# Kernel optimization log

Hardware: AMD Instinct MI355X
Metric: run time of the kernel (lower is better)

## Reference

```python
import jax, jax.numpy as jnp
import numpy as np

N_EMBED = 768
N_HEAD = 12
HEAD_DIM = N_EMBED // N_HEAD


def setup_inputs() -> dict:
    key = jax.random.key(0)
    k1, k2, k3, k4, k5 = jax.random.split(key, 5)
    B, T = 8, 1024
    x = jax.random.normal(k1, (B, T, N_EMBED), dtype=jnp.float32)
    s = 0.02
    W_attn = jax.random.normal(k2, (N_EMBED, 3 * N_EMBED), dtype=jnp.float32) * s
    b_attn = jnp.zeros((3 * N_EMBED,), dtype=jnp.float32)
    W_proj = jax.random.normal(k3, (N_EMBED, N_EMBED), dtype=jnp.float32) * s
    b_proj = jnp.zeros((N_EMBED,), dtype=jnp.float32)
    return {"x": x, "W_attn": W_attn, "b_attn": b_attn, "W_proj": W_proj, "b_proj": b_proj}


def reference(x, W_attn, b_attn, W_proj, b_proj):
    B, T, C = x.shape
    qkv = x @ W_attn + b_attn  # [B, T, 3C]
    q, k, v = jnp.split(qkv, 3, axis=-1)
    # [B, H, T, D]
    q = q.reshape(B, T, N_HEAD, HEAD_DIM).transpose(0, 2, 1, 3)
    k = k.reshape(B, T, N_HEAD, HEAD_DIM).transpose(0, 2, 1, 3)
    v = v.reshape(B, T, N_HEAD, HEAD_DIM).transpose(0, 2, 1, 3)
    scale = 1.0 / jnp.sqrt(jnp.asarray(HEAD_DIM, dtype=x.dtype))
    att = jnp.einsum('bhqd,bhkd->bhqk', q, k) * scale  # [B, H, T, T]
    causal = jnp.tril(jnp.ones((T, T), dtype=bool))
    att = jnp.where(causal[None, None], att, -jnp.inf)
    att = jax.nn.softmax(att, axis=-1)
    y = jnp.einsum('bhqk,bhkd->bhqd', att, v)  # [B, H, T, D]
    y = y.transpose(0, 2, 1, 3).reshape(B, T, C)
    return y @ W_proj + b_proj
```

## Files before the change

kernel.cpp:

```cpp
#include <hip/hip_runtime.h>

#define B_ 8
#define T_ 1024
#define C_ 768
#define H_ 12
#define D_ 64
#define M_ (B_*T_)
#define N3_ (3*C_)
#define NQK_ 1536

#define QSCALE 0.18033688011112042f
#define SXQ (127.0f/6.0f)
#define SWQ (127.0f/0.12f)
#define DEQ ((6.0f/127.0f)*(0.12f/127.0f))

typedef __bf16 bf16x8 __attribute__((ext_vector_type(8)));
typedef float f32x4 __attribute__((ext_vector_type(4)));
typedef int i32x4 __attribute__((ext_vector_type(4)));

__device__ __forceinline__ ushort f2bf(float f){
  __bf16 h = (__bf16)f;
  return __builtin_bit_cast(ushort, h);
}
__device__ __forceinline__ signed char q8(float f, float s){
  float v = rintf(f * s);
  v = fminf(fmaxf(v, -127.f), 127.f);
  return (signed char)(int)v;
}

__device__ __forceinline__ void gload_lds16(const void* g, void* l){
  __builtin_amdgcn_global_load_lds(
      (const __attribute__((address_space(1))) void*)g,
      (__attribute__((address_space(3))) void*)l, 16, 0, 0);
}

__global__ __launch_bounds__(256) void prep(const float* __restrict__ x, signed char* __restrict__ xq,
                     const float* __restrict__ Wa, signed char* __restrict__ Waq,
                     const float* __restrict__ Wp, ushort* __restrict__ WpT){
  const int bid = blockIdx.x, tid = threadIdx.x;
  if (bid < 1536){
    int i = (bid * 256 + tid) * 16;
    union { signed char c[16]; int4 v; } u;
    #pragma unroll
    for (int j = 0; j < 4; ++j){
      float4 f = *(const float4*)(x + i + j*4);
      u.c[j*4+0] = q8(f.x, SXQ); u.c[j*4+1] = q8(f.y, SXQ);
      u.c[j*4+2] = q8(f.z, SXQ); u.c[j*4+3] = q8(f.w, SXQ);
    }
    *(int4*)(xq + i) = u.v;
  } else if (bid < 3264){
    __shared__ float tile[32][33];
    int b2 = bid - 1536;
    int c0 = (b2 % 72) * 32, r0 = (b2 / 72) * 32;
    const int tx = tid & 31, ty = tid >> 5;
    for (int i = ty; i < 32; i += 8)
      tile[i][tx] = Wa[(size_t)(r0 + i) * N3_ + c0 + tx];
    __syncthreads();
    for (int i = ty; i < 32; i += 8)
      Waq[(size_t)(c0 + i) * C_ + r0 + tx] = q8(tile[tx][i], SWQ);
  } else {
    __shared__ float tile[32][33];
    int b2 = bid - 3264;
    int c0 = (b2 % 24) * 32, r0 = (b2 / 24) * 32;
    const int tx = tid & 31, ty = tid >> 5;
    for (int i = ty; i < 32; i += 8)
      tile[i][tx] = Wp[(size_t)(r0 + i) * C_ + c0 + tx];
    __syncthreads();
    for (int i = ty; i < 32; i += 8)
      WpT[(size_t)(c0 + i) * C_ + r0 + tx] = f2bf(tile[tx][i]);
  }
}

__global__ __launch_bounds__(256) void gemm_qkv_i8(const signed char* __restrict__ A,
                        const signed char* __restrict__ BT, const float* __restrict__ bias,
                        ushort* __restrict__ qk, ushort* __restrict__ Vt){
  __shared__ __align__(16) char smem8[34816];
  const int K = C_;
  const int tid = threadIdx.x;
  const int lane = tid & 63, w = tid >> 6;
  const int wr = w >> 1, wc = w & 1;
  const int lr = lane & 15, lg = lane >> 4;
  const int gdx = gridDim.x;
  const int total = gdx * gridDim.y;
  int id = blockIdx.y * gdx + blockIdx.x;
  int nid = (id & 7) * (total >> 3) + (id >> 3);
  const int m0 = (nid / gdx) * 128, n0 = (nid % gdx) * 128;
  i32x4 acc[4][4] = {};
  #define STAGE8(bf, k0s)                                                      \
    _Pragma("unroll")                                                          \
    for (int j = 0; j < 2; ++j){                                               \
      int idj = tid + j * 256;                                                 \
      int row = idj >> 2, sl = idj & 3;                                        \
      gload_lds16(&A [(size_t)(m0 + row) * K + (k0s) + sl * 16],               \
                  &smem8[(bf)*16384 + idj * 16]);                              \
      gload_lds16(&BT[(size_t)(n0 + row) * K + (k0s) + sl * 16],               \
                  &smem8[(bf)*16384 + 8192 + idj * 16]);                       \
    }
  STAGE8(0, 0)
  int cur = 0;
  for (int k0 = 0; k0 < K; k0 += 64){
    const bool more = (k0 + 64 < K);
    if (more) { STAGE8(cur ^ 1, k0 + 64) }
    __builtin_amdgcn_sched_barrier(0);
    if (more) asm volatile("s_waitcnt vmcnt(4)" ::: "memory");
    else      asm volatile("s_waitcnt vmcnt(0)" ::: "memory");
    __builtin_amdgcn_sched_barrier(0);
    __builtin_amdgcn_s_barrier();
    __builtin_amdgcn_sched_barrier(0);
    const char* Asb = &smem8[cur * 16384];
    const char* Bsb = &smem8[cur * 16384 + 8192];
    i32x4 af[4], bfr[4];
    #pragma unroll
    for (int m = 0; m < 4; ++m)
      af[m]  = *(const i32x4*)&Asb[(wr*64 + m*16 + lr) * 64 + lg * 16];
    #pragma unroll
    for (int n = 0; n < 4; ++n)
      bfr[n] = *(const i32x4*)&Bsb[(wc*64 + n*16 + lr) * 64 + lg * 16];
    __builtin_amdgcn_s_setprio(1);
    #pragma unroll
    for (int m = 0; m < 4; ++m)
      #pragma unroll
      for (int n = 0; n < 4; ++n)
        acc[m][n] = __builtin_amdgcn_mfma_i32_16x16x64_i8(af[m], bfr[n], acc[m][n], 0, 0, 0);
    __builtin_amdgcn_s_setprio(0);
    __builtin_amdgcn_sched_barrier(0);
    __builtin_amdgcn_s_barrier();
    __builtin_amdgcn_sched_barrier(0);
    cur ^= 1;
  }
  #undef STAGE8
  constexpr int LDC = 136;
  ushort* Ts = (ushort*)smem8;
  const bool isV = (n0 >= 2*C_);
  #pragma unroll
  for (int n = 0; n < 4; ++n){
    int cl = wc*64 + n*16 + lr;
    int col = n0 + cl;
    float bv = bias[col];
    float sc = (col < C_) ? QSCALE : 1.0f;
    if (isV){
      int rl = wr*64;
      #pragma unroll
      for (int m = 0; m < 4; ++m){
        ushort4 o;
        #pragma unroll
        for (int i = 0; i < 4; ++i)
          ((ushort*)&o)[i] = f2bf((float)acc[m][n][i] * DEQ + bv);
        *(ushort4*)&Ts[cl * LDC + rl + m*16 + lg*4] = o;
      }
    } else {
      #pragma unroll
      for (int m = 0; m < 4; ++m){
        int rl = wr*64 + m*16 + lg*4;
        #pragma unroll
        for (int i = 0; i < 4; ++i)
          Ts[(rl + i) * LDC + cl] = f2bf(((float)acc[m][n][i] * DEQ + bv) * sc);
      }
    }
  }
  __syncthreads();
  const int bb = m0 >> 10, tt = m0 & 1023;
  #pragma unroll
  for (int it = 0; it < 8; ++it){
    int idx = tid + it * 256;
    int rc = idx >> 4, sg = idx & 15;
    int4 v = *(const int4*)&Ts[rc * LDC + sg * 8];
    if (isV){
      int ch = n0 - 2*C_ + rc;
      int hh = ch >> 6, dd = ch & 63;
      *(int4*)&Vt[((size_t)(bb * H_ + hh) * 64 + dd) * 1024 + tt + sg * 8] = v;
    } else {
      *(int4*)&qk[(size_t)(m0 + rc) * NQK_ + n0 + sg * 8] = v;
    }
  }
}

__global__ __launch_bounds__(256) void gemm_proj(const ushort* __restrict__ A, const ushort* __restrict__ BT,
                        const float* __restrict__ bias, float* __restrict__ Cf32,
                        int M, int N, int K){
  __shared__ __align__(16) ushort smem[32768];
  const int tid = threadIdx.x;
  const int lane = tid & 63, w = tid >> 6;
  const int wr = w >> 1, wc = w & 1;
  const int lr = lane & 15, lg = lane >> 4;
  const int gdx = gridDim.x;
  const int total = gdx * gridDim.y;
  int id = blockIdx.y * gdx + blockIdx.x;
  int nid = (id & 7) * (total >> 3) + (id >> 3);
  const int m0 = (nid / gdx) * 128, n0 = (nid % gdx) * 128;
  f32x4 acc[4][4] = {};
  const int srow = lane >> 3;
  const int sseg = (lane & 7) ^ srow;
  #define STAGE(bf, k0s)                                                       \
    _Pragma("unroll")                                                          \
    for (int c = 0; c < 4; ++c){                                               \
      int row = w*32 + c*8 + srow;                                             \
      gload_lds16(&A [(size_t)(m0 + row) * K + (k0s) + sseg * 8],              \
                  &smem[(bf)*16384 + (w*32 + c*8) * 64]);                      \
      gload_lds16(&BT[(size_t)(n0 + row) * K + (k0s) + sseg * 8],              \
                  &smem[(bf)*16384 + 8192 + (w*32 + c*8) * 64]);               \
    }
  STAGE(0, 0)
  int cur = 0;
  for (int k0 = 0; k0 < K; k0 += 64){
    const bool more = (k0 + 64 < K);
    if (more) { STAGE(cur ^ 1, k0 + 64) }
    __builtin_amdgcn_sched_barrier(0);
    if (more) asm volatile("s_waitcnt vmcnt(8)" ::: "memory");
    else      asm volatile("s_waitcnt vmcnt(0)" ::: "memory");
    __builtin_amdgcn_sched_barrier(0);
    __builtin_amdgcn_s_barrier();
    __builtin_amdgcn_sched_barrier(0);
    const ushort* Asb = &smem[cur * 16384];
    const ushort* Bsb = &smem[cur * 16384 + 8192];
    #pragma unroll
    for (int kk = 0; kk < 64; kk += 32){
      bf16x8 af[4], bfr[4];
      #pragma unroll
      for (int m = 0; m < 4; ++m)
        af[m]  = *(const bf16x8*)&Asb[(wr*64 + m*16 + lr) * 64 + ((kk + lg*8) ^ ((lr & 7) << 3))];
      #pragma unroll
      for (int n = 0; n < 4; ++n)
        bfr[n] = *(const bf16x8*)&Bsb[(wc*64 + n*16 + lr) * 64 + ((kk + lg*8) ^ ((lr & 7) << 3))];
      #pragma unroll
      for (int m = 0; m < 4; ++m)
        #pragma unroll
        for (int n = 0; n < 4; ++n)
          acc[m][n] = __builtin_amdgcn_mfma_f32_16x16x32_bf16(af[m], bfr[n], acc[m][n], 0, 0, 0);
    }
    __builtin_amdgcn_sched_barrier(0);
    __builtin_amdgcn_s_barrier();
    __builtin_amdgcn_sched_barrier(0);
    cur ^= 1;
  }
  #undef STAGE
  #pragma unroll
  for (int n = 0; n < 4; ++n){
    int col = n0 + wc*64 + n*16 + lr;
    float bv = bias[col];
    #pragma unroll
    for (int m = 0; m < 4; ++m){
      int rowb = m0 + wr*64 + m*16 + lg*4;
      #pragma unroll
      for (int i = 0; i < 4; ++i)
        Cf32[(size_t)(rowb + i) * N + col] = acc[m][n][i] + bv;
    }
  }
}

__global__ __launch_bounds__(64, 4) void attn_fused(const ushort* __restrict__ qk,
                        const ushort* __restrict__ Vt, ushort* __restrict__ ya){
  __shared__ __align__(16) ushort Ks[2][4096];
  __shared__ __align__(16) ushort Vs[4096];
  __shared__ __align__(16) ushort Ps[32 * 36];
  const int lane = threadIdx.x & 63;
  const int lr = lane & 15, lg = lane >> 4;
  const int srow = lane >> 3;
  const int sseg = (lane & 7) ^ srow;
  const int bx = blockIdx.x;
  const int xcd = bx & 7, ii = bx >> 3;
  const int hi = ii % 12, s = ii / 12;
  const int bh = xcd * 12 + hi;
  const int b = bh / H_, h = bh % H_;
  const ushort* Kb = qk + (size_t)b * T_ * NQK_ + C_ + h * D_;
  const ushort* Vb = Vt + (size_t)bh * D_ * T_;

  int par = 0;
  for (int hf = 0; hf < 2; ++hf){
    const int qw = hf ? (31 - s) : s;
    bf16x8 qf[2][2];
    #pragma unroll
    for (int n = 0; n < 2; ++n){
      int qr = qw*32 + n*16 + lr;
      const ushort* qp = qk + ((size_t)(b * T_ + qr)) * NQK_ + h * D_;
      #pragma unroll
      for (int kk = 0; kk < 2; ++kk)
        qf[n][kk] = __builtin_bit_cast(bf16x8, *(const int4*)(qp + kk*32 + lg*8));
    }

    f32x4 yacc[4][2] = {};
    float lsum[2] = {0.f, 0.f};
    const int qwmin = qw*32;
    const int nktw = ((qwmin + 31) >> 6) + 1;
    #pragma unroll
    for (int c = 0; c < 8; ++c)
      gload_lds16(&Kb[(size_t)(c*8 + srow) * NQK_ + sseg * 8], &Ks[par][c * 512]);
    for (int kt = 0; kt < nktw; ++kt){
      const bool more = (kt + 1 < nktw);
      #pragma unroll
      for (int c = 0; c < 8; ++c)
        gload_lds16(&Vb[(size_t)(c*8 + srow) * T_ + kt*64 + sseg * 8], &Vs[c * 512]);
      if (more){
        #pragma unroll
        for (int c = 0; c < 8; ++c)
          gload_lds16(&Kb[(size_t)((kt+1)*64 + c*8 + srow) * NQK_ + sseg * 8], &Ks[par ^ 1][c * 512]);
        asm volatile("s_waitcnt vmcnt(16)" ::: "memory");
      } else {
        asm volatile("s_waitcnt vmcnt(8)" ::: "memory");
      }
      __builtin_amdgcn_sched_barrier(0);

      f32x4 st[4][2] = {};
      const ushort* Kc = Ks[par];
      #pragma unroll
      for (int kk = 0; kk < 2; ++kk){
        bf16x8 kf[4];
        #pragma unroll
        for (int m = 0; m < 4; ++m)
          kf[m] = *(const bf16x8*)&Kc[(m*16 + lr) * 64 + ((kk*32 + lg*8) ^ ((lr & 7) << 3))];
        __builtin_amdgcn_s_setprio(1);
        #pragma unroll
        for (int m = 0; m < 4; ++m)
          #pragma unroll
          for (int n = 0; n < 2; ++n)
            st[m][n] = __builtin_amdgcn_mfma_f32_16x16x32_bf16(kf[m], qf[n][kk], st[m][n], 0, 0, 0);
        __builtin_amdgcn_s_setprio(0);
      }

      const bool needmask = (kt*64 + 63 > qwmin);
      #pragma unroll
      for (int kkh = 0; kkh < 2; ++kkh){
        #pragma unroll
        for (int n = 0; n < 2; ++n){
          int q = qwmin + n*16 + lr;
          float ps = 0.f;
          #pragma unroll
          for (int mh = 0; mh < 2; ++mh){
            int m = kkh*2 + mh;
            ushort4 pk;
            #pragma unroll
            for (int i = 0; i < 4; ++i){
              float sv = st[m][n][i];
              if (needmask){
                int key = kt*64 + m*16 + lg*4 + i;
                sv = (key <= q) ? sv : -1e30f;
              }
              float p = __builtin_amdgcn_exp2f(sv);
              ps += p;
              ((ushort*)&pk)[i] = f2bf(p);
            }
            *(ushort4*)&Ps[(n*16 + lr) * 36 + mh*16 + lg*4] = pk;
          }
          lsum[n] += ps;
        }
        if (kkh == 0){
          if (more) asm volatile("s_waitcnt vmcnt(8)" ::: "memory");
          else      asm volatile("s_waitcnt vmcnt(0)" ::: "memory");
          __builtin_amdgcn_sched_barrier(0);
        }
        bf16x8 vf[4], pf[2];
        #pragma unroll
        for (int m = 0; m < 4; ++m)
          vf[m] = *(const bf16x8*)&Vs[(m*16 + lr) * 64 + ((kkh*32 + lg*8) ^ ((lr & 7) << 3))];
        #pragma unroll
        for (int n = 0; n < 2; ++n)
          pf[n] = *(const bf16x8*)&Ps[(n*16 + lr) * 36 + lg*8];
        __builtin_amdgcn_s_setprio(1);
        #pragma unroll
        for (int m = 0; m < 4; ++m)
          #pragma unroll
          for (int n = 0; n < 2; ++n)
            yacc[m][n] = __builtin_amdgcn_mfma_f32_16x16x32_bf16(vf[m], pf[n], yacc[m][n], 0, 0, 0);
        __builtin_amdgcn_s_setprio(0);
      }
      if (more) par ^= 1;
    }
    #pragma unroll
    for (int n = 0; n < 2; ++n){
      lsum[n] += __shfl_xor(lsum[n], 16);
      lsum[n] += __shfl_xor(lsum[n], 32);
    }
    #pragma unroll
    for (int n = 0; n < 2; ++n){
      int q = qw*32 + n*16 + lr;
      float inv = 1.0f / lsum[n];
      #pragma unroll
      for (int m = 0; m < 4; ++m){
        ushort4 o;
        #pragma unroll
        for (int i = 0; i < 4; ++i) ((ushort*)&o)[i] = f2bf(yacc[m][n][i] * inv);
        *(ushort4*)&ya[(size_t)(b * T_ + q) * C_ + h * D_ + m*16 + lg*4] = o;
      }
    }
  }
}

extern "C" void kernel_launch(void* const* d_in, const int* in_sizes, int n_in,
                              void* d_out, int out_size, void* d_ws, size_t ws_size,
                              hipStream_t stream){
  (void)in_sizes; (void)n_in; (void)out_size; (void)ws_size;
  const float* x  = (const float*)d_in[0];
  const float* Wa = (const float*)d_in[1];
  const float* ba = (const float*)d_in[2];
  const float* Wp = (const float*)d_in[3];
  const float* bp = (const float*)d_in[4];
  char* ws = (char*)d_ws;
  signed char* xq  = (signed char*)ws;
  signed char* Waq = (signed char*)(ws + 6291456);
  ushort* ya  = (ushort*)ws;
  ushort* WpT = (ushort*)(ws + 12582912);
  ushort* qkb = (ushort*)(ws + 13762560);
  ushort* Vt  = (ushort*)(ws + 38928384);

  prep<<<dim3(3840), dim3(256), 0, stream>>>(x, xq, Wa, Waq, Wp, WpT);
  gemm_qkv_i8<<<dim3(N3_/128, M_/128), dim3(256), 0, stream>>>(xq, Waq, ba, qkb, Vt);
  attn_fused<<<dim3(96*16), dim3(64), 0, stream>>>(qkb, Vt, ya);
  gemm_proj<<<dim3(C_/128, M_/128), dim3(256), 0, stream>>>(ya, WpT, bp, (float*)d_out, M_, C_, C_);
}
```

Baseline: 90.75 us.

## Drop K double-buffering in attention and compute full P tile before PV

Removes the double-buffered K prefetch so each key tile loads its K and V in the same iteration, with a single K buffer and no parity tracking. The softmax probability tile is now computed for all 64 keys into a wider padded LDS buffer (row stride 72) before the PV matmul, instead of interleaving half-tiles with the V wait. This reduces LDS use and simplifies the wait logic, which may allow more resident blocks. The cost is that K load latency is no longer hidden behind the previous tile's compute.

```diff
diff --git a/kernel.cpp b/kernel.cpp
--- a/kernel.cpp
+++ b/kernel.cpp
@@ -94,7 +94,7 @@
       gload_lds16(&A [(size_t)(m0 + row) * K + (k0s) + sl * 16],               \
                   &smem8[(bf)*16384 + idj * 16]);                              \
       gload_lds16(&BT[(size_t)(n0 + row) * K + (k0s) + sl * 16],               \
-                  &smem8[(bf)*16384 + 8192 + idj * 16]);                       \
+                  &smem8[(bf)*16384 + 8192 + (idj) * 16]);                     \
     }
   STAGE8(0, 0)
   int cur = 0;
@@ -250,9 +250,10 @@
 
 __global__ __launch_bounds__(64, 4) void attn_fused(const ushort* __restrict__ qk,
                         const ushort* __restrict__ Vt, ushort* __restrict__ ya){
-  __shared__ __align__(16) ushort Ks[2][4096];
-  __shared__ __align__(16) ushort Vs[4096];
-  __shared__ __align__(16) ushort Ps[32 * 36];
+  constexpr int LD = 72;
+  __shared__ __align__(16) ushort Ks[64 * 64];
+  __shared__ __align__(16) ushort Vs[64 * 64];
+  __shared__ __align__(16) ushort Ps[32 * LD];
   const int lane = threadIdx.x & 63;
   const int lr = lane & 15, lg = lane >> 4;
   const int srow = lane >> 3;
@@ -265,7 +266,6 @@
   const ushort* Kb = qk + (size_t)b * T_ * NQK_ + C_ + h * D_;
   const ushort* Vb = Vt + (size_t)bh * D_ * T_;
 
-  int par = 0;
   for (int hf = 0; hf < 2; ++hf){
     const int qw = hf ? (31 - s) : s;
     bf16x8 qf[2][2];
@@ -282,32 +282,23 @@
     float lsum[2] = {0.f, 0.f};
     const int qwmin = qw*32;
     const int nktw = ((qwmin + 31) >> 6) + 1;
-    #pragma unroll
-    for (int c = 0; c < 8; ++c)
-      gload_lds16(&Kb[(size_t)(c*8 + srow) * NQK_ + sseg * 8], &Ks[par][c * 512]);
     for (int kt = 0; kt < nktw; ++kt){
-      const bool more = (kt + 1 < nktw);
+      #pragma unroll
+      for (int c = 0; c < 8; ++c)
+        gload_lds16(&Kb[(size_t)(kt*64 + c*8 + srow) * NQK_ + sseg * 8], &Ks[c * 512]);
       #pragma unroll
       for (int c = 0; c < 8; ++c)
         gload_lds16(&Vb[(size_t)(c*8 + srow) * T_ + kt*64 + sseg * 8], &Vs[c * 512]);
-      if (more){
-        #pragma unroll
-        for (int c = 0; c < 8; ++c)
-          gload_lds16(&Kb[(size_t)((kt+1)*64 + c*8 + srow) * NQK_ + sseg * 8], &Ks[par ^ 1][c * 512]);
-        asm volatile("s_waitcnt vmcnt(16)" ::: "memory");
-      } else {
-        asm volatile("s_waitcnt vmcnt(8)" ::: "memory");
-      }
+      asm volatile("s_waitcnt vmcnt(8)" ::: "memory");
       __builtin_amdgcn_sched_barrier(0);
 
       f32x4 st[4][2] = {};
-      const ushort* Kc = Ks[par];
       #pragma unroll
       for (int kk = 0; kk < 2; ++kk){
         bf16x8 kf[4];
         #pragma unroll
         for (int m = 0; m < 4; ++m)
-          kf[m] = *(const bf16x8*)&Kc[(m*16 + lr) * 64 + ((kk*32 + lg*8) ^ ((lr & 7) << 3))];
+          kf[m] = *(const bf16x8*)&Ks[(m*16 + lr) * 64 + ((kk*32 + lg*8) ^ ((lr & 7) << 3))];
         __builtin_amdgcn_s_setprio(1);
         #pragma unroll
         for (int m = 0; m < 4; ++m)
@@ -319,42 +310,40 @@
 
       const bool needmask = (kt*64 + 63 > qwmin);
       #pragma unroll
-      for (int kkh = 0; kkh < 2; ++kkh){
-        #pragma unroll
-        for (int n = 0; n < 2; ++n){
-          int q = qwmin + n*16 + lr;
-          float ps = 0.f;
+      for (int n = 0; n < 2; ++n){
+        int q = qwmin + n*16 + lr;
+        float ps = 0.f;
+        #pragma unroll
+        for (int m = 0; m < 4; ++m){
+          ushort4 pk;
           #pragma unroll
-          for (int mh = 0; mh < 2; ++mh){
-            int m = kkh*2 + mh;
-            ushort4 pk;
-            #pragma unroll
-            for (int i = 0; i < 4; ++i){
-              float sv = st[m][n][i];
-              if (needmask){
-                int key = kt*64 + m*16 + lg*4 + i;
-                sv = (key <= q) ? sv : -1e30f;
-              }
-              float p = __builtin_amdgcn_exp2f(sv);
-              ps += p;
-              ((ushort*)&pk)[i] = f2bf(p);
+          for (int i = 0; i < 4; ++i){
+            float sv = st[m][n][i];
+            if (needmask){
+              int key = kt*64 + m*16 + lg*4 + i;
+              sv = (key <= q) ? sv : -1e30f;
             }
-            *(ushort4*)&Ps[(n*16 + lr) * 36 + mh*16 + lg*4] = pk;
+            float p = __builtin_amdgcn_exp2f(sv);
+            ps += p;
+            ((ushort*)&pk)[i] = f2bf(p);
           }
-          lsum[n] += ps;
+          *(ushort4*)&Ps[(n*16 + lr) * LD + m*16 + lg*4] = pk;
         }
-        if (kkh == 0){
-          if (more) asm volatile("s_waitcnt vmcnt(8)" ::: "memory");
-          else      asm volatile("s_waitcnt vmcnt(0)" ::: "memory");
-          __builtin_amdgcn_sched_barrier(0);
-        }
+        lsum[n] += ps;
+      }
+
+      asm volatile("s_waitcnt vmcnt(0)" ::: "memory");
+      __builtin_amdgcn_sched_barrier(0);
+
+      #pragma unroll
+      for (int kk = 0; kk < 2; ++kk){
         bf16x8 vf[4], pf[2];
         #pragma unroll
         for (int m = 0; m < 4; ++m)
-          vf[m] = *(const bf16x8*)&Vs[(m*16 + lr) * 64 + ((kkh*32 + lg*8) ^ ((lr & 7) << 3))];
+          vf[m] = *(const bf16x8*)&Vs[(m*16 + lr) * 64 + ((kk*32 + lg*8) ^ ((lr & 7) << 3))];
         #pragma unroll
         for (int n = 0; n < 2; ++n)
-          pf[n] = *(const bf16x8*)&Ps[(n*16 + lr) * 36 + lg*8];
+          pf[n] = *(const bf16x8*)&Ps[(n*16 + lr) * LD + kk*32 + lg*8];
         __builtin_amdgcn_s_setprio(1);
         #pragma unroll
         for (int m = 0; m < 4; ++m)
@@ -363,7 +352,6 @@
             yacc[m][n] = __builtin_amdgcn_mfma_f32_16x16x32_bf16(vf[m], pf[n], yacc[m][n], 0, 0, 0);
         __builtin_amdgcn_s_setprio(0);
       }
-      if (more) par ^= 1;
     }
     #pragma unroll
     for (int n = 0; n < 2; ++n){
```

After: 89.81 us. Within noise of the previous version (-1.0%).
